# Performance work log

Hardware: AMD Instinct MI355X
Metric: run time of the kernel (lower is better)

## Reference

```python
import jax, jax.numpy as jnp
import numpy as np
import math

# IPA hyperparameters (AlphaFold2 / ProtSeed defaults)
H, C, PQ, PV = 12, 16, 4, 8
CS, CZ = 384, 128
INF, EPS = 1e5, 1e-8
CAT = H * (CZ + C + 4 * PV)  # 2112


def setup_inputs() -> dict:
    key = jax.random.key(0)
    ks = jax.random.split(key, 20)
    B, N = 1, 512
    s = jax.random.normal(ks[0], (B, N, CS), jnp.float32)
    z = jax.random.normal(ks[1], (B, N, N, CZ), jnp.float32)
    # valid rotation matrices via QR of random gaussians
    rot = jnp.linalg.qr(jax.random.normal(ks[2], (B, N, 3, 3), jnp.float32))[0]
    trans = jax.random.normal(ks[3], (B, N, 3), jnp.float32)
    mask = jnp.ones((B, N), jnp.float32)
    sc = 0.02
    params = {
        'w_q': jax.random.normal(ks[4], (CS, H * C), jnp.float32) * sc,
        'b_q': jnp.zeros((H * C,), jnp.float32),
        'w_kv': jax.random.normal(ks[5], (CS, 2 * H * C), jnp.float32) * sc,
        'b_kv': jnp.zeros((2 * H * C,), jnp.float32),
        'w_qp': jax.random.normal(ks[6], (CS, H * PQ * 3), jnp.float32) * sc,
        'b_qp': jnp.zeros((H * PQ * 3,), jnp.float32),
        'w_kvp': jax.random.normal(ks[7], (CS, H * (PQ + PV) * 3), jnp.float32) * sc,
        'b_kvp': jnp.zeros((H * (PQ + PV) * 3,), jnp.float32),
        'w_b': jax.random.normal(ks[8], (CZ, H), jnp.float32) * sc,
        'b_b': jnp.zeros((H,), jnp.float32),
        'head_weights': jnp.full((H,), 0.5414, jnp.float32),  # softplus^-1(1)
        'w_out': jax.random.normal(ks[9], (CAT, CS), jnp.float32) * sc,
        'b_out': jnp.zeros((CS,), jnp.float32),
    }
    return {'s': s, 'z': z, 'rot': rot, 'trans': trans, 'mask': mask, **params}


def reference(s, z, rot, trans, mask, w_q, b_q, w_kv, b_kv, w_qp, b_qp,
              w_kvp, b_kvp, w_b, b_b, head_weights, w_out, b_out):
    B, N, _ = s.shape
    w_c = math.sqrt(1.0 / (3 * C))
    w_l = math.sqrt(1.0 / 3)
    w_p = math.sqrt(1.0 / (3 * (PQ * 9.0 / 2)))

    # scalar q/k/v: [B,N,H,C]
    q = (s @ w_q + b_q).reshape(B, N, H, C)
    kv = (s @ w_kv + b_kv).reshape(B, N, H, 2 * C)
    k, v = kv[..., :C], kv[..., C:]

    # point q/k/v in global frame. torch splits the projection into 3 chunks
    # (x,y,z) along the channel dim then stacks -> [B,N,H*P,3]
    def to_pts(w, b, p):
        pts = jnp.stack(jnp.split(s @ w + b, 3, axis=-1), axis=-1)  # [B,N,H*p,3]
        pts = jnp.einsum('bnij,bnpj->bnpi', rot, pts) + trans[:, :, None, :]
        return pts.reshape(B, N, H, p, 3)

    q_pts = to_pts(w_qp, b_qp, PQ)
    kv_pts = to_pts(w_kvp, b_kvp, PQ + PV)
    k_pts, v_pts = kv_pts[..., :PQ, :], kv_pts[..., PQ:, :]

    # pair bias [B,N,N,H]
    bias = z @ w_b + b_b

    # scalar attention logits [B,H,i,j]
    a = jnp.einsum('bihc,bjhc->bhij', q, k) * w_c
    a = a + w_l * jnp.transpose(bias, (0, 3, 1, 2))

    # point-distance term: [B,i,j,H,PQ]
    d2 = jnp.sum((q_pts[:, :, None] - k_pts[:, None]) ** 2, axis=-1)
    hw = jax.nn.softplus(head_weights) * w_p
    pt_att = -0.5 * jnp.sum(d2 * hw[None, None, None, :, None], axis=-1)  # [B,i,j,H]
    a = a + jnp.transpose(pt_att, (0, 3, 1, 2))

    sq_mask = INF * (mask[:, :, None] * mask[:, None, :] - 1.0)  # [B,i,j]
    a = jax.nn.softmax(a + sq_mask[:, None], axis=-1)  # [B,H,i,j]

    # scalar output [B,N,H*C]
    o = jnp.einsum('bhij,bjhc->bihc', a, v).reshape(B, N, H * C)

    # point output, mapped back to local frames: [B,i,H,PV,3]
    o_pt = jnp.einsum('bhij,bjhpx->bihpx', a, v_pts)
    o_pt = jnp.einsum('bnji,bnhpj->bnhpi', rot, o_pt - trans[:, :, None, None, :])
    o_pt_norm = jnp.sqrt(jnp.sum(o_pt ** 2, axis=-1) + EPS).reshape(B, N, H * PV)
    o_pt = o_pt.reshape(B, N, H * PV, 3)

    # pair output [B,N,H*CZ]
    o_pair = jnp.einsum('bhij,bijc->bihc', a, z).reshape(B, N, H * CZ)

    cat = jnp.concatenate(
        [o, o_pt[..., 0], o_pt[..., 1], o_pt[..., 2], o_pt_norm, o_pair], axis=-1)
    return cat @ w_out + b_out  # [B,N,C_s]
```

## Files before the change

### kernel.cpp

```cpp
#include <hip/hip_runtime.h>
#include <math.h>

#define NN 512
#define CSd 384
#define CATd 2112
#define KF_CHUNK 264
#define KF_SPLIT 8

__global__ void k_projgemm(const float* __restrict__ s,
                           const float* __restrict__ w_q, const float* __restrict__ b_q,
                           const float* __restrict__ w_kv, const float* __restrict__ b_kv,
                           const float* __restrict__ w_qp, const float* __restrict__ b_qp,
                           const float* __restrict__ w_kvp, const float* __restrict__ b_kvp,
                           float* __restrict__ proj)
{
  __shared__ float sT[384 * 40];
  const int t  = threadIdx.x;
  const int i0 = blockIdx.x * 32;
  const int c0 = blockIdx.y * 64;

  for (int u = t; u < 32 * 384; u += 256) {
    int row = u / 384, col = u % 384;
    sT[col * 40 + row] = s[(i0 + row) * CSd + col];
  }
  __syncthreads();

  const int c    = t & 63;
  const int rgrp = t >> 6;
  const int gc   = c0 + c;

  const float* wp;
  int stride;
  float bias;
  if (gc < 192)      { wp = w_q   + gc;         stride = 192; bias = b_q[gc]; }
  else if (gc < 576) { wp = w_kv  + (gc - 192); stride = 384; bias = b_kv[gc - 192]; }
  else if (gc < 720) { wp = w_qp  + (gc - 576); stride = 144; bias = b_qp[gc - 576]; }
  else               { wp = w_kvp + (gc - 720); stride = 432; bias = b_kvp[gc - 720]; }

  float acc[8];
#pragma unroll
  for (int j = 0; j < 8; j++) acc[j] = bias;

  const int r0 = rgrp * 8;
#pragma unroll 4
  for (int kk = 0; kk < 384; kk++) {
    float wv = *wp; wp += stride;
    const float4 a0 = *reinterpret_cast<const float4*>(&sT[kk * 40 + r0]);
    const float4 a1 = *reinterpret_cast<const float4*>(&sT[kk * 40 + r0 + 4]);
    acc[0] += a0.x * wv; acc[1] += a0.y * wv; acc[2] += a0.z * wv; acc[3] += a0.w * wv;
    acc[4] += a1.x * wv; acc[5] += a1.y * wv; acc[6] += a1.z * wv; acc[7] += a1.w * wv;
  }
#pragma unroll
  for (int j = 0; j < 8; j++)
    proj[(size_t)(i0 + r0 + j) * 1152 + gc] = acc[j];
}

__global__ void k_rot(const float* __restrict__ proj,
                      const float* __restrict__ rot, const float* __restrict__ trans,
                      float* __restrict__ q, float* __restrict__ kT, float* __restrict__ vcatT,
                      float* __restrict__ qp, float* __restrict__ kpT)
{
  __shared__ float ptsL[576];
  const int i = blockIdx.x, t = threadIdx.x;
  const float* pr = proj + (size_t)i * 1152;

  for (int u = t; u < 576; u += 256) ptsL[u] = pr[576 + u];

  for (int cI = t; cI < 576; cI += 256) {
    float pv = pr[cI];
    if (cI < 192) q[i * 192 + cI] = pv;
    else {
      int local = cI - 192, h = local >> 5, cc = local & 31;
      if (cc < 16) kT[(size_t)(h * 16 + cc) * NN + i] = pv;
      else         vcatT[(size_t)(h * 16 + (cc - 16)) * NN + i] = pv;
    }
  }
  __syncthreads();

  for (int p = t; p < 192; p += 256) {
    float x, y, zz;
    if (p < 48) { x = ptsL[p]; y = ptsL[48 + p]; zz = ptsL[96 + p]; }
    else { int idx = p - 48; x = ptsL[144 + idx]; y = ptsL[288 + idx]; zz = ptsL[432 + idx]; }
    const float* Rm = rot + i * 9;
    const float* tr = trans + i * 3;
    float rx = Rm[0] * x + Rm[1] * y + Rm[2] * zz + tr[0];
    float ry = Rm[3] * x + Rm[4] * y + Rm[5] * zz + tr[1];
    float rz = Rm[6] * x + Rm[7] * y + Rm[8] * zz + tr[2];
    if (p < 48) {
      float* d = qp + ((size_t)i * 48 + p) * 3;
      d[0] = rx; d[1] = ry; d[2] = rz;
    } else {
      int idx = p - 48, h = idx / 12, pp = idx % 12;
      if (pp < 4) {
        size_t rbase = (size_t)((h * 4 + pp) * 3) * NN + i;
        kpT[rbase] = rx; kpT[rbase + NN] = ry; kpT[rbase + 2 * NN] = rz;
      } else {
        size_t rbase = (size_t)(192 + (h * 8 + pp - 4) * 3) * NN + i;
        vcatT[rbase] = rx; vcatT[rbase + NN] = ry; vcatT[rbase + 2 * NN] = rz;
      }
    }
  }
}

__global__ void __launch_bounds__(512)
k_fused(const float* __restrict__ z, const float* __restrict__ w_b,
        const float* __restrict__ b_b, const float* __restrict__ mask,
        const float* __restrict__ q, const float* __restrict__ kT,
        const float* __restrict__ qp, const float* __restrict__ kpT,
        const float* __restrict__ hws, const float* __restrict__ vcatT,
        const float* __restrict__ rot, const float* __restrict__ trans,
        float* __restrict__ cat)
{
  __shared__ float PL[12 * 513];
  __shared__ float red[4][32][49];
  __shared__ float qL[192], qpL[144], hwL[12];
  __shared__ float optF[288];

  const int i = blockIdx.x, t = threadIdx.x;
  const int w = t >> 6, l = t & 63;

  if (t < 192) qL[t] = q[i * 192 + t];
  else if (t < 336) qpL[t - 192] = qp[(size_t)i * 144 + (t - 192)];
  else if (t < 348) hwL[t - 336] = 0.13608276348f * log1pf(expf(hws[t - 336]));
  __syncthreads();

  {
    const int j = t;
    float acc[12];
#pragma unroll
    for (int h = 0; h < 12; h++) acc[h] = 0.f;

    const float4* zr = reinterpret_cast<const float4*>(z + ((size_t)i * NN + j) * 128);
#pragma unroll
    for (int b4 = 0; b4 < 4; b4++) {
      float4 zv[8];
#pragma unroll
      for (int u = 0; u < 8; u++) zv[u] = zr[b4 * 8 + u];
#pragma unroll
      for (int u = 0; u < 8; u++) {
        const int c0 = b4 * 32 + u * 4;
#pragma unroll
        for (int h = 0; h < 12; h++) {
          acc[h] += zv[u].x * w_b[(c0 + 0) * 12 + h]
                  + zv[u].y * w_b[(c0 + 1) * 12 + h]
                  + zv[u].z * w_b[(c0 + 2) * 12 + h]
                  + zv[u].w * w_b[(c0 + 3) * 12 + h];
        }
      }
    }

    const float mterm = 100000.0f * (mask[i] * mask[j] - 1.0f);
    const float W_L = 0.57735026919f;
    const float W_C = 0.14433756730f;
#pragma unroll 4
    for (int h = 0; h < 12; h++) {
      float dot = 0.f;
#pragma unroll
      for (int c = 0; c < 16; c++)
        dot += qL[h * 16 + c] * kT[(size_t)(h * 16 + c) * NN + j];
      float d2 = 0.f;
#pragma unroll
      for (int pc = 0; pc < 12; pc++) {
        float dd = qpL[h * 12 + pc] - kpT[(size_t)(h * 12 + pc) * NN + j];
        d2 += dd * dd;
      }
      PL[h * 513 + j] = W_L * (acc[h] + b_b[h]) + mterm + W_C * dot - 0.5f * hwL[h] * d2;
    }
  }
  __syncthreads();

  for (int h = w; h < 12; h += 8) {
    float x[8];
    float m = -1e30f;
#pragma unroll
    for (int k = 0; k < 8; k++) { x[k] = PL[h * 513 + k * 64 + l]; m = fmaxf(m, x[k]); }
    for (int o = 1; o < 64; o <<= 1) m = fmaxf(m, __shfl_xor(m, o));
    float sm = 0.f;
#pragma unroll
    for (int k = 0; k < 8; k++) { x[k] = expf(x[k] - m); sm += x[k]; }
    for (int o = 1; o < 64; o <<= 1) sm += __shfl_xor(sm, o);
    float inv = 1.0f / sm;
#pragma unroll
    for (int k = 0; k < 8; k++) PL[h * 513 + k * 64 + l] = x[k] * inv;
  }
  __syncthreads();

  for (int v = w; v < 480; v += 8) {
    const int h = (v < 192) ? (v >> 4) : ((v - 192) / 24);
    const float* vr = vcatT + (size_t)v * NN;
    const float* pr = PL + h * 513;
    float acc = 0.f;
#pragma unroll
    for (int k = 0; k < 8; k++)
      acc += pr[k * 64 + l] * vr[k * 64 + l];
    for (int o = 1; o < 64; o <<= 1) acc += __shfl_xor(acc, o);
    if (l == 0) {
      if (v < 192) cat[(size_t)i * CATd + v] = acc;
      else         optF[v - 192] = acc;
    }
  }

  {
    const int sub = (t >> 5) & 1;
    const int c4  = t & 31;
    const int jq  = t >> 6;
    float acc[12][4];
#pragma unroll
    for (int h = 0; h < 12; h++)
#pragma unroll
      for (int c = 0; c < 4; c++) acc[h][c] = 0.f;

    const float4* zb = reinterpret_cast<const float4*>(z) +
                       ((size_t)i * NN + jq * 64 + sub) * 32 + c4;
    const float* prow = PL + jq * 64 + sub;
    for (int step = 0; step < 32; step++) {
      const float4 zv = zb[(size_t)step * 64];
      const int jo = step * 2;
#pragma unroll
      for (int h = 0; h < 12; h++) {
        const float pv = prow[h * 513 + jo];
        acc[h][0] += pv * zv.x; acc[h][1] += pv * zv.y;
        acc[h][2] += pv * zv.z; acc[h][3] += pv * zv.w;
      }
    }
#pragma unroll
    for (int h = 0; h < 12; h++)
#pragma unroll
      for (int c = 0; c < 4; c++)
        acc[h][c] += __shfl_xor(acc[h][c], 32);

    if (jq >= 4 && sub == 0) {
#pragma unroll
      for (int h = 0; h < 12; h++)
#pragma unroll
        for (int c = 0; c < 4; c++) red[jq - 4][c4][h * 4 + c] = acc[h][c];
    }
    __syncthreads();
    if (jq < 4 && sub == 0) {
#pragma unroll
      for (int h = 0; h < 12; h++)
#pragma unroll
        for (int c = 0; c < 4; c++) red[jq][c4][h * 4 + c] += acc[h][c];
    }
    __syncthreads();

    for (int e = t; e < 1536; e += 512) {
      const int h = e >> 7, c = e & 127, ci = c >> 2, cc = c & 3;
      float sv = red[0][ci][h * 4 + cc] + red[1][ci][h * 4 + cc]
               + red[2][ci][h * 4 + cc] + red[3][ci][h * 4 + cc];
      cat[(size_t)i * CATd + 576 + e] = sv;
    }
  }

  if (t < 96) {
    const int h = t >> 3, p = t & 7;
    const float* Rm = rot + i * 9;
    const float* tr = trans + i * 3;
    float ox = optF[(h * 8 + p) * 3 + 0] - tr[0];
    float oy = optF[(h * 8 + p) * 3 + 1] - tr[1];
    float oz = optF[(h * 8 + p) * 3 + 2] - tr[2];
    float rx = Rm[0] * ox + Rm[3] * oy + Rm[6] * oz;
    float ry = Rm[1] * ox + Rm[4] * oy + Rm[7] * oz;
    float rz = Rm[2] * ox + Rm[5] * oy + Rm[8] * oz;
    float nrm = sqrtf(rx * rx + ry * ry + rz * rz + 1e-8f);
    size_t b = (size_t)i * CATd;
    cat[b + 192 + t] = rx; cat[b + 288 + t] = ry;
    cat[b + 384 + t] = rz; cat[b + 480 + t] = nrm;
  }
}

__global__ void k_final(const float* __restrict__ cat, const float* __restrict__ w_out,
                        float* __restrict__ part)
{
  __shared__ float sT[KF_CHUNK * 36];
  const int t  = threadIdx.x;
  const int i0 = blockIdx.x * 32;
  const int c0 = blockIdx.y * 64;
  const int k0 = blockIdx.z * KF_CHUNK;

  for (int u = t; u < 32 * KF_CHUNK; u += 256) {
    int row = u / KF_CHUNK, kk = u % KF_CHUNK;
    sT[kk * 36 + row] = cat[(size_t)(i0 + row) * CATd + k0 + kk];
  }
  __syncthreads();

  const int c    = t & 63;
  const int rgrp = t >> 6;
  const int r0   = rgrp * 8;
  const int gc   = c0 + c;

  float acc[8];
#pragma unroll
  for (int j = 0; j < 8; j++) acc[j] = 0.f;

  const float* wp = w_out + (size_t)k0 * 384 + gc;
#pragma unroll 4
  for (int kk = 0; kk < KF_CHUNK; kk++) {
    float wv = wp[(size_t)kk * 384];
    const float4 a0 = *reinterpret_cast<const float4*>(&sT[kk * 36 + r0]);
    const float4 a1 = *reinterpret_cast<const float4*>(&sT[kk * 36 + r0 + 4]);
    acc[0] += a0.x * wv; acc[1] += a0.y * wv; acc[2] += a0.z * wv; acc[3] += a0.w * wv;
    acc[4] += a1.x * wv; acc[5] += a1.y * wv; acc[6] += a1.z * wv; acc[7] += a1.w * wv;
  }

  float* pb = part + (size_t)blockIdx.z * NN * 384;
#pragma unroll
  for (int j = 0; j < 8; j++)
    pb[(size_t)(i0 + r0 + j) * 384 + gc] = acc[j];
}

__global__ void k_reduce(const float* __restrict__ part, const float* __restrict__ b_out,
                         float* __restrict__ out)
{
  const int idx = blockIdx.x * 256 + threadIdx.x;
  const int c = idx % 384;
  float acc = b_out[c];
#pragma unroll
  for (int ks = 0; ks < KF_SPLIT; ks++)
    acc += part[(size_t)ks * NN * 384 + idx];
  out[idx] = acc;
}

extern "C" void kernel_launch(void* const* d_in, const int* in_sizes, int n_in,
                              void* d_out, int out_size, void* d_ws, size_t ws_size,
                              hipStream_t stream) {
  const float* s      = (const float*)d_in[0];
  const float* z      = (const float*)d_in[1];
  const float* rot    = (const float*)d_in[2];
  const float* trans  = (const float*)d_in[3];
  const float* mask   = (const float*)d_in[4];
  const float* w_q    = (const float*)d_in[5];
  const float* b_q    = (const float*)d_in[6];
  const float* w_kv   = (const float*)d_in[7];
  const float* b_kv   = (const float*)d_in[8];
  const float* w_qp   = (const float*)d_in[9];
  const float* b_qp   = (const float*)d_in[10];
  const float* w_kvp  = (const float*)d_in[11];
  const float* b_kvp  = (const float*)d_in[12];
  const float* w_b    = (const float*)d_in[13];
  const float* b_b    = (const float*)d_in[14];
  const float* hws    = (const float*)d_in[15];
  const float* w_out  = (const float*)d_in[16];
  const float* b_out  = (const float*)d_in[17];
  float* out = (float*)d_out;

  float* ws    = (float*)d_ws;
  float* q     = ws;
  float* kT    = q     + 98304;
  float* vcatT = kT    + 98304;
  float* qp    = vcatT + 245760;
  float* kpT   = qp    + 73728;
  float* scratch = kpT + 73728;
  float* cat   = scratch + 3145728;
  float* proj  = scratch;
  float* part  = scratch;

  k_projgemm<<<dim3(16, 18), 256, 0, stream>>>(s, w_q, b_q, w_kv, b_kv,
                                               w_qp, b_qp, w_kvp, b_kvp, proj);
  k_rot<<<512, 256, 0, stream>>>(proj, rot, trans, q, kT, vcatT, qp, kpT);
  k_fused<<<512, 512, 0, stream>>>(z, w_b, b_b, mask, q, kT, qp, kpT, hws,
                                   vcatT, rot, trans, cat);
  k_final<<<dim3(16, 6, KF_SPLIT), 256, 0, stream>>>(cat, w_out, part);
  k_reduce<<<768, 256, 0, stream>>>(part, b_out, out);
}
```

Measured before the change: 215.2 us.

## Split fused attention kernel across two head groups per row

The fused attention kernel now launches a second grid dimension, with each block handling 6 of the 12 heads for one query row. Shared memory and register accumulators are halved, which should raise occupancy and double the number of blocks available to fill the GPU. The cost is that each z row is read twice, once per head group, for both the bias projection and the pair-output accumulation.

```diff
diff --git a/kernel.cpp b/kernel.cpp
--- a/kernel.cpp
+++ b/kernel.cpp
@@ -111,24 +111,26 @@
         const float* __restrict__ rot, const float* __restrict__ trans,
         float* __restrict__ cat)
 {
-  __shared__ float PL[12 * 513];
-  __shared__ float red[4][32][49];
-  __shared__ float qL[192], qpL[144], hwL[12];
-  __shared__ float optF[288];
-
-  const int i = blockIdx.x, t = threadIdx.x;
-  const int w = t >> 6, l = t & 63;
-
-  if (t < 192) qL[t] = q[i * 192 + t];
-  else if (t < 336) qpL[t - 192] = qp[(size_t)i * 144 + (t - 192)];
-  else if (t < 348) hwL[t - 336] = 0.13608276348f * log1pf(expf(hws[t - 336]));
+  __shared__ float PL[6 * 513];
+  __shared__ float red[4][32][25];
+  __shared__ float qL[96], qpL[72], hwL[6];
+  __shared__ float optF[144];
+
+  const int i  = blockIdx.x, t = threadIdx.x;
+  const int hh = blockIdx.y;
+  const int hb = hh * 6;
+  const int w  = t >> 6, l = t & 63;
+
+  if (t < 96) qL[t] = q[i * 192 + hb * 16 + t];
+  else if (t < 168) qpL[t - 96] = qp[(size_t)i * 144 + hb * 12 + (t - 96)];
+  else if (t < 174) hwL[t - 168] = 0.13608276348f * log1pf(expf(hws[hb + t - 168]));
   __syncthreads();
 
   {
     const int j = t;
-    float acc[12];
-#pragma unroll
-    for (int h = 0; h < 12; h++) acc[h] = 0.f;
+    float acc[6];
+#pragma unroll
+    for (int h = 0; h < 6; h++) acc[h] = 0.f;
 
     const float4* zr = reinterpret_cast<const float4*>(z + ((size_t)i * NN + j) * 128);
 #pragma unroll
@@ -140,11 +142,11 @@
       for (int u = 0; u < 8; u++) {
         const int c0 = b4 * 32 + u * 4;
 #pragma unroll
-        for (int h = 0; h < 12; h++) {
-          acc[h] += zv[u].x * w_b[(c0 + 0) * 12 + h]
-                  + zv[u].y * w_b[(c0 + 1) * 12 + h]
-                  + zv[u].z * w_b[(c0 + 2) * 12 + h]
-                  + zv[u].w * w_b[(c0 + 3) * 12 + h];
+        for (int h = 0; h < 6; h++) {
+          acc[h] += zv[u].x * w_b[(c0 + 0) * 12 + hb + h]
+                  + zv[u].y * w_b[(c0 + 1) * 12 + hb + h]
+                  + zv[u].z * w_b[(c0 + 2) * 12 + hb + h]
+                  + zv[u].w * w_b[(c0 + 3) * 12 + hb + h];
         }
       }
     }
@@ -152,24 +154,25 @@
     const float mterm = 100000.0f * (mask[i] * mask[j] - 1.0f);
     const float W_L = 0.57735026919f;
     const float W_C = 0.14433756730f;
-#pragma unroll 4
-    for (int h = 0; h < 12; h++) {
+#pragma unroll 2
+    for (int h = 0; h < 6; h++) {
       float dot = 0.f;
 #pragma unroll
       for (int c = 0; c < 16; c++)
-        dot += qL[h * 16 + c] * kT[(size_t)(h * 16 + c) * NN + j];
+        dot += qL[h * 16 + c] * kT[(size_t)((hb + h) * 16 + c) * NN + j];
       float d2 = 0.f;
 #pragma unroll
       for (int pc = 0; pc < 12; pc++) {
-        float dd = qpL[h * 12 + pc] - kpT[(size_t)(h * 12 + pc) * NN + j];
+        float dd = qpL[h * 12 + pc] - kpT[(size_t)((hb + h) * 12 + pc) * NN + j];
         d2 += dd * dd;
       }
-      PL[h * 513 + j] = W_L * (acc[h] + b_b[h]) + mterm + W_C * dot - 0.5f * hwL[h] * d2;
-    }
-  }
-  __syncthreads();
-
-  for (int h = w; h < 12; h += 8) {
+      PL[h * 513 + j] = W_L * (acc[h] + b_b[hb + h]) + mterm + W_C * dot - 0.5f * hwL[h] * d2;
+    }
+  }
+  __syncthreads();
+
+  if (w < 6) {
+    const int h = w;
     float x[8];
     float m = -1e30f;
 #pragma unroll
@@ -185,18 +188,20 @@
   }
   __syncthreads();
 
-  for (int v = w; v < 480; v += 8) {
-    const int h = (v < 192) ? (v >> 4) : ((v - 192) / 24);
-    const float* vr = vcatT + (size_t)v * NN;
-    const float* pr = PL + h * 513;
+  for (int vv = w; vv < 240; vv += 8) {
+    int hl, vrow;
+    if (vv < 96) { hl = vv >> 4; vrow = hb * 16 + vv; }
+    else { int u = vv - 96; hl = u / 24; vrow = 192 + hb * 24 + u; }
+    const float* vr = vcatT + (size_t)vrow * NN;
+    const float* pr = PL + hl * 513;
     float acc = 0.f;
 #pragma unroll
     for (int k = 0; k < 8; k++)
       acc += pr[k * 64 + l] * vr[k * 64 + l];
     for (int o = 1; o < 64; o <<= 1) acc += __shfl_xor(acc, o);
     if (l == 0) {
-      if (v < 192) cat[(size_t)i * CATd + v] = acc;
-      else         optF[v - 192] = acc;
+      if (vv < 96) cat[(size_t)i * CATd + hb * 16 + vv] = acc;
+      else         optF[vv - 96] = acc;
     }
   }
 
@@ -204,9 +209,9 @@
     const int sub = (t >> 5) & 1;
     const int c4  = t & 31;
     const int jq  = t >> 6;
-    float acc[12][4];
-#pragma unroll
-    for (int h = 0; h < 12; h++)
+    float acc[6][4];
+#pragma unroll
+    for (int h = 0; h < 6; h++)
 #pragma unroll
       for (int c = 0; c < 4; c++) acc[h][c] = 0.f;
 
@@ -217,53 +222,53 @@
       const float4 zv = zb[(size_t)step * 64];
       const int jo = step * 2;
 #pragma unroll
-      for (int h = 0; h < 12; h++) {
+      for (int h = 0; h < 6; h++) {
         const float pv = prow[h * 513 + jo];
         acc[h][0] += pv * zv.x; acc[h][1] += pv * zv.y;
         acc[h][2] += pv * zv.z; acc[h][3] += pv * zv.w;
       }
     }
 #pragma unroll
-    for (int h = 0; h < 12; h++)
+    for (int h = 0; h < 6; h++)
 #pragma unroll
       for (int c = 0; c < 4; c++)
         acc[h][c] += __shfl_xor(acc[h][c], 32);
 
     if (jq >= 4 && sub == 0) {
 #pragma unroll
-      for (int h = 0; h < 12; h++)
+      for (int h = 0; h < 6; h++)
 #pragma unroll
         for (int c = 0; c < 4; c++) red[jq - 4][c4][h * 4 + c] = acc[h][c];
     }
     __syncthreads();
     if (jq < 4 && sub == 0) {
 #pragma unroll
-      for (int h = 0; h < 12; h++)
+      for (int h = 0; h < 6; h++)
 #pragma unroll
         for (int c = 0; c < 4; c++) red[jq][c4][h * 4 + c] += acc[h][c];
     }
     __syncthreads();
 
-    for (int e = t; e < 1536; e += 512) {
+    for (int e = t; e < 768; e += 512) {
       const int h = e >> 7, c = e & 127, ci = c >> 2, cc = c & 3;
       float sv = red[0][ci][h * 4 + cc] + red[1][ci][h * 4 + cc]
                + red[2][ci][h * 4 + cc] + red[3][ci][h * 4 + cc];
-      cat[(size_t)i * CATd + 576 + e] = sv;
-    }
-  }
-
-  if (t < 96) {
-    const int h = t >> 3, p = t & 7;
+      cat[(size_t)i * CATd + 576 + (size_t)(hb + h) * 128 + c] = sv;
+    }
+  }
+
+  if (t < 48) {
+    const int hl = t >> 3, p = t & 7;
     const float* Rm = rot + i * 9;
     const float* tr = trans + i * 3;
-    float ox = optF[(h * 8 + p) * 3 + 0] - tr[0];
-    float oy = optF[(h * 8 + p) * 3 + 1] - tr[1];
-    float oz = optF[(h * 8 + p) * 3 + 2] - tr[2];
+    float ox = optF[hl * 24 + p * 3 + 0] - tr[0];
+    float oy = optF[hl * 24 + p * 3 + 1] - tr[1];
+    float oz = optF[hl * 24 + p * 3 + 2] - tr[2];
     float rx = Rm[0] * ox + Rm[3] * oy + Rm[6] * oz;
     float ry = Rm[1] * ox + Rm[4] * oy + Rm[7] * oz;
     float rz = Rm[2] * ox + Rm[5] * oy + Rm[8] * oz;
     float nrm = sqrtf(rx * rx + ry * ry + rz * rz + 1e-8f);
-    size_t b = (size_t)i * CATd;
+    size_t b = (size_t)i * CATd + hb * 8;
     cat[b + 192 + t] = rx; cat[b + 288 + t] = ry;
     cat[b + 384 + t] = rz; cat[b + 480 + t] = nrm;
   }
@@ -358,8 +363,8 @@
   k_projgemm<<<dim3(16, 18), 256, 0, stream>>>(s, w_q, b_q, w_kv, b_kv,
                                                w_qp, b_qp, w_kvp, b_kvp, proj);
   k_rot<<<512, 256, 0, stream>>>(proj, rot, trans, q, kT, vcatT, qp, kpT);
-  k_fused<<<512, 512, 0, stream>>>(z, w_b, b_b, mask, q, kT, qp, kpT, hws,
-                                   vcatT, rot, trans, cat);
+  k_fused<<<dim3(512, 2), 512, 0, stream>>>(z, w_b, b_b, mask, q, kT, qp, kpT, hws,
+                                            vcatT, rot, trans, cat);
   k_final<<<dim3(16, 6, KF_SPLIT), 256, 0, stream>>>(cat, w_out, part);
   k_reduce<<<768, 256, 0, stream>>>(part, b_out, out);
 }
```

Result: slower. 220.8 us (+2.6%).
